# Kernel tuning notes

Measured on AMD Instinct MI355X. Metric: run time of the kernel, lower is better.

## Reference

```python
import jax, jax.numpy as jnp
import numpy as np

B, CQ, CKV, E = 8, 256, 256, 256
H, W = 64, 64
HP, WP = 32, 32


def setup_inputs() -> dict:
    key = jax.random.key(0)
    ks = jax.random.split(key, 6)
    C = jax.random.normal(ks[0], (B, CQ, H, W), dtype=jnp.float32)
    P = jax.random.normal(ks[1], (B, CKV, HP, WP), dtype=jnp.float32)
    # 1x1 conv weights, kaiming-ish scale; stored as [out_ch, in_ch]
    theta_w = jax.random.normal(ks[2], (E, CQ), dtype=jnp.float32) * (1.0 / np.sqrt(CQ))
    phi_w = jax.random.normal(ks[3], (E, CKV), dtype=jnp.float32) * (1.0 / np.sqrt(CKV))
    g_w = jax.random.normal(ks[4], (E, CKV), dtype=jnp.float32) * (1.0 / np.sqrt(CKV))
    out_w = jax.random.normal(ks[5], (CQ, E), dtype=jnp.float32) * (1.0 / np.sqrt(E))
    return {"C": C, "P": P, "theta_w": theta_w, "phi_w": phi_w, "g_w": g_w, "out_w": out_w}


def reference(C, P, theta_w, phi_w, g_w, out_w):
    b, _, h, w = C.shape
    e = theta_w.shape[0]
    # 1x1 convs are channel GEMMs
    theta_C = jnp.einsum('bchw,ec->behw', C, theta_w).reshape(b, e, h * w)   # [B,E,Nq]
    phi_P = jnp.einsum('bchw,ec->behw', P, phi_w).reshape(b, e, -1)          # [B,E,Nkv]
    g_P = jnp.einsum('bchw,ec->behw', P, g_w).reshape(b, e, -1)              # [B,E,Nkv]
    attn = jnp.einsum('ben,bem->bnm', theta_C, phi_P) / (e ** 0.5)           # [B,Nq,Nkv]
    attn = jax.nn.softmax(attn, axis=-1)
    out = jnp.einsum('bem,bnm->ben', g_P, attn).reshape(b, e, h, w)          # [B,E,H,W]
    out = jnp.einsum('behw,ce->bchw', out, out_w)                            # [B,CQ,H,W]
    return jnp.concatenate([C, out], axis=1)
```

## Files before the change

kernel.cpp:

```cpp
#include <hip/hip_runtime.h>


typedef __attribute__((ext_vector_type(8))) short short8;
typedef __attribute__((ext_vector_type(16))) float f32x16;
typedef unsigned short ushort_t;

__device__ __forceinline__ unsigned short f2bf(float f) {
    unsigned int u = __float_as_uint(f);
    u += 0x7FFFu + ((u >> 16) & 1u);
    return (unsigned short)(u >> 16);
}
__device__ __forceinline__ unsigned int pack2bf(float a, float b) {
    return (unsigned int)f2bf(a) | ((unsigned int)f2bf(b) << 16);
}
__device__ __forceinline__ void gload16(const ushort_t* g, ushort_t* l) {
    __builtin_amdgcn_global_load_lds(
        (const __attribute__((address_space(1))) unsigned int*)g,
        (__attribute__((address_space(3))) unsigned int*)l, 16, 0, 0);
}
__device__ __forceinline__ f32x16 zero16() {
    f32x16 z;
#pragma unroll
    for (int i = 0; i < 16; ++i) z[i] = 0.f;
    return z;
}

__global__ __launch_bounds__(256) void prep_all(const float* __restrict__ P,
                                                const float* __restrict__ C,
                                                const float* __restrict__ thw,
                                                const float* __restrict__ phw,
                                                const float* __restrict__ ow,
                                                const float* __restrict__ gw,
                                                ushort_t* __restrict__ pT,
                                                ushort_t* __restrict__ cT,
                                                ushort_t* __restrict__ thc,
                                                ushort_t* __restrict__ phc,
                                                ushort_t* __restrict__ w2c) {
    int blk = blockIdx.x;
    int t = threadIdx.x;
    __shared__ float Xs[64][68];
    if (blk < 2560) {
        const float* X;
        ushort_t* xT;
        int N, bx, by, b;
        if (blk < 512) {
            X = P; xT = pT; N = 1024;
            bx = blk & 15; by = (blk >> 4) & 3; b = blk >> 6;
        } else {
            int r = blk - 512;
            X = C; xT = cT; N = 4096;
            bx = r & 63; by = (r >> 6) & 3; b = r >> 8;
        }
        int n0 = bx * 64, c0 = by * 64;
        const float* Xb = X + ((size_t)b * 256 + c0) * N + n0;
        int cl = t >> 4, nl = (t & 15) * 4;
#pragma unroll
        for (int ci = 0; ci < 4; ++ci) {
            int c = ci * 16 + cl;
            *(float4*)&Xs[c][nl] = *(const float4*)(Xb + (size_t)c * N + nl);
        }
        __syncthreads();
        ushort_t* xb = xT + (size_t)b * ((size_t)N * 256);
        int nl2 = t & 63, cgb = t >> 6;
#pragma unroll
        for (int cp = 0; cp < 2; ++cp) {
            int cg = cp * 4 + cgb;
            int cb = c0 + cg * 8;
            int n = n0 + nl2;
            short8 v;
#pragma unroll
            for (int u = 0; u < 8; ++u) v[u] = (short)f2bf(Xs[cg * 8 + u][nl2]);
            size_t i16 = ((size_t)(n >> 5) * 16 + (cb >> 4)) * 64 + ((cb >> 3) & 1) * 32 + (n & 31);
            *(short8*)(xb + i16 * 8) = v;
        }
    } else if (blk < 3072) {
        int r = blk - 2560;
        int which = r >> 8;
        int e = r & 255, c = t;
        const float* src = which ? phw : thw;
        ushort_t* dst = which ? phc : thc;
        int idx = ((((e >> 5) * 16 + (c >> 4)) * 64 + ((c >> 3) & 1) * 32 + (e & 31)) << 3) + (c & 7);
        dst[idx] = f2bf(src[e * 256 + c]);
    } else {
        int c0 = (blk - 3072) * 8;
        float acc[8] = {};
        for (int e = 0; e < 256; ++e) {
            float g = gw[e * 256 + t];
#pragma unroll
            for (int i = 0; i < 8; ++i) acc[i] += ow[(c0 + i) * 256 + e] * g;
        }
#pragma unroll
        for (int i = 0; i < 8; ++i) {
            int c = c0 + i, k = t;
            int idx = ((((c >> 5) * 16 + (k >> 4)) * 64 + ((k >> 3) & 1) * 32 + (c & 31)) << 3) + (k & 7);
            w2c[idx] = f2bf(acc[i]);
        }
    }
}

__global__ __launch_bounds__(128, 2) void proj_mfma(const ushort_t* __restrict__ thc,
                                                    const ushort_t* __restrict__ phc,
                                                    const ushort_t* __restrict__ w2c,
                                                    const ushort_t* __restrict__ cT,
                                                    const ushort_t* __restrict__ pT,
                                                    ushort_t* __restrict__ thetaA,
                                                    ushort_t* __restrict__ phiA,
                                                    ushort_t* __restrict__ gVx) {
    int blk = blockIdx.x;
    int tid = threadIdx.x, lane = tid & 63, wid = tid >> 6;
    int l31 = lane & 31, lh = lane >> 5;
    int role, b, nt;
    const ushort_t *Wc, *xTb;
    ushort_t* outp;
    float scale = 1.f;
    if (blk < 512) {
        role = 0; b = blk & 7; nt = blk >> 3;
        Wc = thc; xTb = cT + (size_t)b * 1048576; outp = thetaA + (size_t)b * 1048576;
        scale = 1.4426950408889634f / 16.0f;
    } else if (blk < 640) {
        int r = blk - 512; role = 1; b = r & 7; nt = r >> 3;
        Wc = phc; xTb = pT + (size_t)b * 262144; outp = phiA + (size_t)b * 262144;
    } else {
        int r = blk - 640; role = 2; b = r & 7; nt = r >> 3;
        Wc = w2c; xTb = pT + (size_t)b * 262144; outp = gVx + (size_t)b * 262144;
    }
    const int n0 = nt * 64 + wid * 32;
    const int ncr = (n0 >> 5) * 16;

    f32x16 o[8];
#pragma unroll
    for (int f = 0; f < 8; ++f) o[f] = zero16();

#pragma unroll
    for (int ks = 0; ks < 16; ++ks) {
        short8 xf = *(const short8*)(xTb + ((size_t)(ncr + ks) * 64 + lane) * 8);
#pragma unroll
        for (int f = 0; f < 8; ++f) {
            short8 wf = *(const short8*)(Wc + ((size_t)(f * 16 + ks) * 64 + lane) * 8);
            o[f] = __builtin_amdgcn_mfma_f32_32x32x16_bf16(wf, xf, o[f], 0, 0, 0);
        }
    }

    if (role < 2) {
#pragma unroll
        for (int f = 0; f < 8; ++f) {
#pragma unroll
            for (int rq = 0; rq < 4; ++rq) {
                uint2 st;
                st.x = pack2bf(o[f][4 * rq + 0] * scale, o[f][4 * rq + 1] * scale);
                st.y = pack2bf(o[f][4 * rq + 2] * scale, o[f][4 * rq + 3] * scale);
                size_t addr = ((size_t)(ncr + f * 2 + (rq >> 1)) * 64 + l31 + 32 * (rq & 1)) * 8 + 4 * lh;
                *(uint2*)(outp + addr) = st;
            }
        }
    } else {
        int kvq = (n0 >> 4) + (l31 >> 4);
        int lhw = 32 * ((l31 >> 3) & 1);
        int kl = l31 & 7;
#pragma unroll
        for (int f = 0; f < 8; ++f) {
#pragma unroll
            for (int r2 = 0; r2 < 16; ++r2) {
                int crow = (r2 & 3) + 8 * (r2 >> 2) + 4 * lh;
                size_t addr = ((size_t)(f * 64 + kvq) * 64 + crow + lhw) * 8 + kl;
                outp[addr] = f2bf(o[f][r2]);
            }
        }
    }
}

__global__ __launch_bounds__(512, 2) void attn7(const ushort_t* __restrict__ thetaA,
                                                const ushort_t* __restrict__ phiA,
                                                const ushort_t* __restrict__ gVx,
                                                const float* __restrict__ Cf,
                                                float* __restrict__ out) {
    const int b = blockIdx.x & 7, qt = blockIdx.x >> 3;
    const int tid = threadIdx.x, lane = tid & 63, wid = tid >> 6;
    const int l31 = lane & 31, lh = lane >> 5;
    const int h = wid >> 2, qg = wid & 3;

    __shared__ __align__(16) ushort_t smem[65536];
    __shared__ float rlS[4][32];

    const ushort_t* thA = thetaA + (size_t)b * 1048576;
    const ushort_t* phA = phiA + (size_t)b * 262144;
    const ushort_t* gVb = gVx + (size_t)b * 262144;

    auto stageK = [&](int j) {
        if ((wid & 2) == 0) {
            int hh = wid >> 2;
            const ushort_t* src = phA + (size_t)(2 * j + hh) * 8192 + (wid & 1) * 4096 + lane * 8;
            ushort_t* dst = smem + hh * 16384 + (j & 1) * 8192 + (wid & 1) * 4096;
#pragma unroll
            for (int i = 0; i < 8; ++i) gload16(src + i * 512, dst + i * 512);
        }
    };
    auto stageV = [&](int j) {
        if ((wid & 2) == 2) {
            int hh = wid >> 2;
#pragma unroll
            for (int cg2 = 0; cg2 < 4; ++cg2) {
                int cg = (wid & 1) * 4 + cg2;
#pragma unroll
                for (int jj = 0; jj < 2; ++jj) {
                    const ushort_t* src =
                        gVb + ((size_t)(cg * 64 + 4 * j + 2 * hh + jj) * 64 + lane) * 8;
                    ushort_t* dst = smem + 32768 + hh * 16384 + (j & 1) * 8192 + cg * 1024 + jj * 512;
                    gload16(src, dst);
                }
            }
        }
    };

    stageK(0); stageK(1); stageV(0);

    short8 qf[16];
    {
        const int qcr = (qt * 4 + qg) * 16;
#pragma unroll
        for (int ks = 0; ks < 16; ++ks)
            qf[ks] = *(const short8*)(thA + ((size_t)(qcr + ks) * 64 + lane) * 8);
    }

    f32x16 o[8];
#pragma unroll
    for (int f = 0; f < 8; ++f) o[f] = zero16();
    float rl = 0.f;

    const size_t cbase = (size_t)b * 1048576 + (size_t)qt * 128 + (size_t)l31 * 4;
    const size_t dofs = (size_t)b * 1048576;
    size_t cpo = 0;
    float4 cpv;

    asm volatile("s_waitcnt vmcnt(0)" ::: "memory");
    __builtin_amdgcn_s_barrier();
    __builtin_amdgcn_sched_barrier(0);

    f32x16 s = zero16();
    {
        const ushort_t* Kb = smem + h * 16384;
#pragma unroll
        for (int ks = 0; ks < 16; ++ks) {
            short8 kf = *(const short8*)(Kb + (size_t)ks * 512 + lane * 8);
            s = __builtin_amdgcn_mfma_f32_32x32x16_bf16(kf, qf[ks], s, 0, 0, 0);
        }
    }

    for (int it = 0; it < 16; ++it) {
        asm volatile("s_waitcnt vmcnt(0)" ::: "memory");
        __builtin_amdgcn_s_barrier();
        __builtin_amdgcn_sched_barrier(0);
        if (it < 14) stageK(it + 2);
        if (it < 15) stageV(it + 1);

        if (it > 0) *(float4*)(out + cpo + dofs) = cpv;
        cpo = cbase + (size_t)(it * 16 + 2 * wid + lh) * 4096;
        cpv = *(const float4*)(Cf + cpo);

        float ps = 0.f;
#pragma unroll
        for (int r = 0; r < 16; ++r) {
            s[r] = __builtin_amdgcn_exp2f(s[r]);
            ps += s[r];
        }
        ps += __shfl_xor(ps, 32);
        rl += ps;

        unsigned int a0 = pack2bf(s[0], s[1]),   b0 = pack2bf(s[4], s[5]);
        unsigned int a1 = pack2bf(s[2], s[3]),   b1 = pack2bf(s[6], s[7]);
        unsigned int a2 = pack2bf(s[8], s[9]),   b2 = pack2bf(s[12], s[13]);
        unsigned int a3 = pack2bf(s[10], s[11]), b3 = pack2bf(s[14], s[15]);
        asm volatile("v_permlane32_swap_b32 %0, %1" : "+v"(a0), "+v"(b0));
        asm volatile("v_permlane32_swap_b32 %0, %1" : "+v"(a1), "+v"(b1));
        asm volatile("v_permlane32_swap_b32 %0, %1" : "+v"(a2), "+v"(b2));
        asm volatile("v_permlane32_swap_b32 %0, %1" : "+v"(a3), "+v"(b3));
        union PW { unsigned int u[4]; short8 v; };
        PW p0; p0.u[0] = a0; p0.u[1] = a1; p0.u[2] = b0; p0.u[3] = b1;
        PW p1; p1.u[0] = a2; p1.u[1] = a3; p1.u[2] = b2; p1.u[3] = b3;

        const ushort_t* Vb = smem + 32768 + h * 16384 + (it & 1) * 8192;
        const ushort_t* Kb = smem + h * 16384 + ((it + 1) & 1) * 8192;
        __builtin_amdgcn_s_setprio(1);
        if (it < 15) {
            f32x16 sn = zero16();
#pragma unroll
            for (int ks2 = 0; ks2 < 2; ++ks2) {
                short8 pf = ks2 ? p1.v : p0.v;
#pragma unroll
                for (int f = 0; f < 8; ++f) {
                    short8 vf = *(const short8*)(Vb + (size_t)f * 1024 + ks2 * 512 + lane * 8);
                    o[f] = __builtin_amdgcn_mfma_f32_32x32x16_bf16(vf, pf, o[f], 0, 0, 0);
                    int ks = ks2 * 8 + f;
                    short8 kf = *(const short8*)(Kb + (size_t)ks * 512 + lane * 8);
                    sn = __builtin_amdgcn_mfma_f32_32x32x16_bf16(kf, qf[ks], sn, 0, 0, 0);
                }
            }
            s = sn;
        } else {
#pragma unroll
            for (int ks2 = 0; ks2 < 2; ++ks2) {
                short8 pf = ks2 ? p1.v : p0.v;
#pragma unroll
                for (int f = 0; f < 8; ++f) {
                    short8 vf = *(const short8*)(Vb + (size_t)f * 1024 + ks2 * 512 + lane * 8);
                    o[f] = __builtin_amdgcn_mfma_f32_32x32x16_bf16(vf, pf, o[f], 0, 0, 0);
                }
            }
        }
        __builtin_amdgcn_s_setprio(0);
        __builtin_amdgcn_sched_barrier(0);
    }

    *(float4*)(out + cpo + dofs) = cpv;

    __syncthreads();

    if (wid >= 4) {
        float* part = (float*)smem + (size_t)(wid - 4) * 8192;
#pragma unroll
        for (int f = 0; f < 8; ++f)
#pragma unroll
            for (int r = 0; r < 16; ++r) {
                int e = f * 32 + (r & 3) + 8 * (r >> 2) + 4 * lh;
                part[e * 32 + l31] = o[f][r];
            }
        if (lane < 32) rlS[wid - 4][l31] = rl;
    }
    __syncthreads();
    if (wid < 4) {
        float inv = 1.f / (rl + rlS[wid][l31]);
        const float* part = (const float*)smem + (size_t)wid * 8192;
        float* ob = out + (size_t)b * 2097152 + (size_t)256 * 4096 + qt * 128 + qg * 32 + l31;
#pragma unroll
        for (int f = 0; f < 8; ++f)
#pragma unroll
            for (int r = 0; r < 16; ++r) {
                int e = f * 32 + (r & 3) + 8 * (r >> 2) + 4 * lh;
                ob[(size_t)e * 4096] = (o[f][r] + part[e * 32 + l31]) * inv;
            }
    }
}


extern "C" void kernel_launch(void* const* d_in, const int* in_sizes, int n_in,
                              void* d_out, int out_size, void* d_ws, size_t ws_size,
                              hipStream_t stream) {
    const float* C       = (const float*)d_in[0];
    const float* P       = (const float*)d_in[1];
    const float* theta_w = (const float*)d_in[2];
    const float* phi_w   = (const float*)d_in[3];
    const float* g_w     = (const float*)d_in[4];
    const float* out_w   = (const float*)d_in[5];
    float* out = (float*)d_out;

    ushort_t* ws = (ushort_t*)d_ws;
    ushort_t* thetaA = ws;
    ushort_t* cT     = ws + 8388608;
    ushort_t* phiA   = ws + 16777216;
    ushort_t* pT     = ws + 18874368;
    ushort_t* gVx    = ws + 20971520;
    ushort_t* thWc   = ws + 23068672;
    ushort_t* phWc   = ws + 23134208;
    ushort_t* w2c    = ws + 23199744;

    prep_all<<<3104, 256, 0, stream>>>(P, C, theta_w, phi_w, out_w, g_w,
                                       pT, cT, thWc, phWc, w2c);
    proj_mfma<<<768, 128, 0, stream>>>(thWc, phWc, w2c, cT, pT, thetaA, phiA, gVx);
    attn7<<<256, 512, 0, stream>>>(thetaA, phiA, gVx, C, out);
}
```

Before: 117.6 us.

## Fuse activation transpose and bf16 conversion into projection GEMM kernel

The separate pass that transposed C and P into bf16 MFMA-fragment layout in global memory is removed. The projection kernel now loads a 256x64 fp32 tile of the raw input into shared memory and packs bf16 fragments on the fly. Blocks grow to 256 threads, with four waves splitting the query and embedding dimensions. This avoids writing and re-reading a full bf16 copy of both inputs, at the cost of about 68KB of LDS per block, which limits occupancy, and some strided LDS reads.

```diff
diff --git a/kernel.cpp b/kernel.cpp
--- a/kernel.cpp
+++ b/kernel.cpp
@@ -25,64 +25,24 @@
     return z;
 }
 
-__global__ __launch_bounds__(256) void prep_all(const float* __restrict__ P,
-                                                const float* __restrict__ C,
-                                                const float* __restrict__ thw,
-                                                const float* __restrict__ phw,
-                                                const float* __restrict__ ow,
-                                                const float* __restrict__ gw,
-                                                ushort_t* __restrict__ pT,
-                                                ushort_t* __restrict__ cT,
-                                                ushort_t* __restrict__ thc,
-                                                ushort_t* __restrict__ phc,
-                                                ushort_t* __restrict__ w2c) {
+__global__ __launch_bounds__(256) void prep_w(const float* __restrict__ thw,
+                                              const float* __restrict__ phw,
+                                              const float* __restrict__ ow,
+                                              const float* __restrict__ gw,
+                                              ushort_t* __restrict__ thc,
+                                              ushort_t* __restrict__ phc,
+                                              ushort_t* __restrict__ w2c) {
     int blk = blockIdx.x;
     int t = threadIdx.x;
-    __shared__ float Xs[64][68];
-    if (blk < 2560) {
-        const float* X;
-        ushort_t* xT;
-        int N, bx, by, b;
-        if (blk < 512) {
-            X = P; xT = pT; N = 1024;
-            bx = blk & 15; by = (blk >> 4) & 3; b = blk >> 6;
-        } else {
-            int r = blk - 512;
-            X = C; xT = cT; N = 4096;
-            bx = r & 63; by = (r >> 6) & 3; b = r >> 8;
-        }
-        int n0 = bx * 64, c0 = by * 64;
-        const float* Xb = X + ((size_t)b * 256 + c0) * N + n0;
-        int cl = t >> 4, nl = (t & 15) * 4;
-#pragma unroll
-        for (int ci = 0; ci < 4; ++ci) {
-            int c = ci * 16 + cl;
-            *(float4*)&Xs[c][nl] = *(const float4*)(Xb + (size_t)c * N + nl);
-        }
-        __syncthreads();
-        ushort_t* xb = xT + (size_t)b * ((size_t)N * 256);
-        int nl2 = t & 63, cgb = t >> 6;
-#pragma unroll
-        for (int cp = 0; cp < 2; ++cp) {
-            int cg = cp * 4 + cgb;
-            int cb = c0 + cg * 8;
-            int n = n0 + nl2;
-            short8 v;
-#pragma unroll
-            for (int u = 0; u < 8; ++u) v[u] = (short)f2bf(Xs[cg * 8 + u][nl2]);
-            size_t i16 = ((size_t)(n >> 5) * 16 + (cb >> 4)) * 64 + ((cb >> 3) & 1) * 32 + (n & 31);
-            *(short8*)(xb + i16 * 8) = v;
-        }
-    } else if (blk < 3072) {
-        int r = blk - 2560;
-        int which = r >> 8;
-        int e = r & 255, c = t;
+    if (blk < 512) {
+        int which = blk >> 8;
+        int e = blk & 255, c = t;
         const float* src = which ? phw : thw;
         ushort_t* dst = which ? phc : thc;
         int idx = ((((e >> 5) * 16 + (c >> 4)) * 64 + ((c >> 3) & 1) * 32 + (e & 31)) << 3) + (c & 7);
         dst[idx] = f2bf(src[e * 256 + c]);
     } else {
-        int c0 = (blk - 3072) * 8;
+        int c0 = (blk - 512) * 8;
         float acc[8] = {};
         for (int e = 0; e < 256; ++e) {
             float g = gw[e * 256 + t];
@@ -98,57 +58,82 @@
     }
 }
 
-__global__ __launch_bounds__(128, 2) void proj_mfma(const ushort_t* __restrict__ thc,
-                                                    const ushort_t* __restrict__ phc,
-                                                    const ushort_t* __restrict__ w2c,
-                                                    const ushort_t* __restrict__ cT,
-                                                    const ushort_t* __restrict__ pT,
-                                                    ushort_t* __restrict__ thetaA,
-                                                    ushort_t* __restrict__ phiA,
-                                                    ushort_t* __restrict__ gVx) {
+__global__ __launch_bounds__(256, 2) void proj_all(const ushort_t* __restrict__ thc,
+                                                   const ushort_t* __restrict__ phc,
+                                                   const ushort_t* __restrict__ w2c,
+                                                   const float* __restrict__ C,
+                                                   const float* __restrict__ P,
+                                                   ushort_t* __restrict__ thetaA,
+                                                   ushort_t* __restrict__ phiA,
+                                                   ushort_t* __restrict__ gVx) {
+    __shared__ float Xs[256][68];
     int blk = blockIdx.x;
     int tid = threadIdx.x, lane = tid & 63, wid = tid >> 6;
     int l31 = lane & 31, lh = lane >> 5;
-    int role, b, nt;
-    const ushort_t *Wc, *xTb;
+    const int wq = wid & 1, we = wid >> 1;
+
+    int role, b, nt, N;
+    const ushort_t* Wc;
+    const float* Xg;
     ushort_t* outp;
     float scale = 1.f;
     if (blk < 512) {
         role = 0; b = blk & 7; nt = blk >> 3;
-        Wc = thc; xTb = cT + (size_t)b * 1048576; outp = thetaA + (size_t)b * 1048576;
-        scale = 1.4426950408889634f / 16.0f;
+        Wc = thc; Xg = C + (size_t)b * 1048576; outp = thetaA + (size_t)b * 1048576;
+        N = 4096; scale = 1.4426950408889634f / 16.0f;
     } else if (blk < 640) {
         int r = blk - 512; role = 1; b = r & 7; nt = r >> 3;
-        Wc = phc; xTb = pT + (size_t)b * 262144; outp = phiA + (size_t)b * 262144;
+        Wc = phc; Xg = P + (size_t)b * 262144; outp = phiA + (size_t)b * 262144;
+        N = 1024;
     } else {
         int r = blk - 640; role = 2; b = r & 7; nt = r >> 3;
-        Wc = w2c; xTb = pT + (size_t)b * 262144; outp = gVx + (size_t)b * 262144;
-    }
-    const int n0 = nt * 64 + wid * 32;
+        Wc = w2c; Xg = P + (size_t)b * 262144; outp = gVx + (size_t)b * 262144;
+        N = 1024;
+    }
+
+    {
+        const float* Xb = Xg + nt * 64;
+#pragma unroll
+        for (int i = 0; i < 16; ++i) {
+            int idx = i * 256 + tid;
+            int row = idx >> 4, c4 = (idx & 15) * 4;
+            *(float4*)&Xs[row][c4] = *(const float4*)(Xb + (size_t)row * N + c4);
+        }
+    }
+    __syncthreads();
+
+    const int n0 = nt * 64 + wq * 32;
     const int ncr = (n0 >> 5) * 16;
-
-    f32x16 o[8];
-#pragma unroll
-    for (int f = 0; f < 8; ++f) o[f] = zero16();
+    const int q = wq * 32 + l31;
+
+    f32x16 o[4];
+#pragma unroll
+    for (int f = 0; f < 4; ++f) o[f] = zero16();
 
 #pragma unroll
     for (int ks = 0; ks < 16; ++ks) {
-        short8 xf = *(const short8*)(xTb + ((size_t)(ncr + ks) * 64 + lane) * 8);
-#pragma unroll
-        for (int f = 0; f < 8; ++f) {
+        const int cb = ks * 16 + lh * 8;
+        union PW { unsigned int u[4]; short8 v; } xw;
+#pragma unroll
+        for (int j = 0; j < 4; ++j)
+            xw.u[j] = pack2bf(Xs[cb + 2 * j][q], Xs[cb + 2 * j + 1][q]);
+#pragma unroll
+        for (int f2 = 0; f2 < 4; ++f2) {
+            int f = we * 4 + f2;
             short8 wf = *(const short8*)(Wc + ((size_t)(f * 16 + ks) * 64 + lane) * 8);
-            o[f] = __builtin_amdgcn_mfma_f32_32x32x16_bf16(wf, xf, o[f], 0, 0, 0);
+            o[f2] = __builtin_amdgcn_mfma_f32_32x32x16_bf16(wf, xw.v, o[f2], 0, 0, 0);
         }
     }
 
     if (role < 2) {
 #pragma unroll
-        for (int f = 0; f < 8; ++f) {
+        for (int f2 = 0; f2 < 4; ++f2) {
+            int f = we * 4 + f2;
 #pragma unroll
             for (int rq = 0; rq < 4; ++rq) {
                 uint2 st;
-                st.x = pack2bf(o[f][4 * rq + 0] * scale, o[f][4 * rq + 1] * scale);
-                st.y = pack2bf(o[f][4 * rq + 2] * scale, o[f][4 * rq + 3] * scale);
+                st.x = pack2bf(o[f2][4 * rq + 0] * scale, o[f2][4 * rq + 1] * scale);
+                st.y = pack2bf(o[f2][4 * rq + 2] * scale, o[f2][4 * rq + 3] * scale);
                 size_t addr = ((size_t)(ncr + f * 2 + (rq >> 1)) * 64 + l31 + 32 * (rq & 1)) * 8 + 4 * lh;
                 *(uint2*)(outp + addr) = st;
             }
@@ -158,12 +143,13 @@
         int lhw = 32 * ((l31 >> 3) & 1);
         int kl = l31 & 7;
 #pragma unroll
-        for (int f = 0; f < 8; ++f) {
+        for (int f2 = 0; f2 < 4; ++f2) {
+            int f = we * 4 + f2;
 #pragma unroll
             for (int r2 = 0; r2 < 16; ++r2) {
                 int crow = (r2 & 3) + 8 * (r2 >> 2) + 4 * lh;
                 size_t addr = ((size_t)(f * 64 + kvq) * 64 + crow + lhw) * 8 + kl;
-                outp[addr] = f2bf(o[f][r2]);
+                outp[addr] = f2bf(o[f2][r2]);
             }
         }
     }
@@ -355,16 +341,13 @@
 
     ushort_t* ws = (ushort_t*)d_ws;
     ushort_t* thetaA = ws;
-    ushort_t* cT     = ws + 8388608;
-    ushort_t* phiA   = ws + 16777216;
-    ushort_t* pT     = ws + 18874368;
-    ushort_t* gVx    = ws + 20971520;
-    ushort_t* thWc   = ws + 23068672;
-    ushort_t* phWc   = ws + 23134208;
-    ushort_t* w2c    = ws + 23199744;
-
-    prep_all<<<3104, 256, 0, stream>>>(P, C, theta_w, phi_w, out_w, g_w,
-                                       pT, cT, thWc, phWc, w2c);
-    proj_mfma<<<768, 128, 0, stream>>>(thWc, phWc, w2c, cT, pT, thetaA, phiA, gVx);
+    ushort_t* phiA   = ws + 8388608;
+    ushort_t* gVx    = ws + 10485760;
+    ushort_t* thWc   = ws + 12582912;
+    ushort_t* phWc   = ws + 12648448;
+    ushort_t* w2c    = ws + 12713984;
+
+    prep_w<<<544, 256, 0, stream>>>(theta_w, phi_w, out_w, g_w, thWc, phWc, w2c);
+    proj_all<<<768, 256, 0, stream>>>(thWc, phWc, w2c, C, P, thetaA, phiA, gVx);
     attn7<<<256, 512, 0, stream>>>(thetaA, phiA, gVx, C, out);
 }
```

After: 111.6 us. 1.05x faster.
